# Kernel tuning notes

Hardware: AMD Instinct MI355X
Metric: run time of the kernel (lower is better)

The kernel has to match this reference:

```python
import jax, jax.numpy as jnp
import numpy as np

B, N, C = 64, 16384, 3
NUM_PATCHES, PATCH_POINTS, EMBED_DIM = 64, 32, 384
BN_EPS = 1e-5


def farthest_point_sample(xyz, npoint):
    # xyz: (B, N, 3) -> (B, npoint) int32 indices. Deterministic start at index 0
    # (torch version uses a random start point).
    b, n, _ = xyz.shape
    bidx = jnp.arange(b)

    def step(carry, _):
        distance, farthest = carry
        centroid = xyz[bidx, farthest][:, None, :]          # (B,1,3)
        d = jnp.sum((xyz - centroid) ** 2, -1)              # (B,N)
        distance = jnp.minimum(distance, d)
        nxt = jnp.argmax(distance, -1).astype(jnp.int32)
        return (distance, nxt), farthest

    init = (jnp.full((b, n), 1e10, xyz.dtype), jnp.zeros((b,), jnp.int32))
    _, cent = jax.lax.scan(step, init, None, length=npoint)
    return jnp.transpose(cent)                               # (B, npoint)


def query_ball(xyz, new_xyz, nsample):
    # nsample nearest neighbors by squared distance (radius arg is unused in source).
    sq = (jnp.sum(new_xyz ** 2, -1)[:, :, None]
          + jnp.sum(xyz ** 2, -1)[:, None, :]
          - 2.0 * jnp.einsum('bsc,bnc->bsn', new_xyz, xyz))  # (B,S,N)
    _, idx = jax.lax.top_k(-sq, nsample)                     # smallest distances
    return idx                                               # (B,S,K)


def batchnorm(h, g, b):
    # training-mode BN over (batch*patches, points) per channel (last axis)
    m = jnp.mean(h, axis=(0, 1, 2))
    v = jnp.mean((h - m) ** 2, axis=(0, 1, 2))
    return (h - m) * jax.lax.rsqrt(v + BN_EPS) * g + b


def setup_inputs() -> dict:
    key = jax.random.key(0)
    ks = jax.random.split(key, 4)
    x = jax.random.normal(ks[0], (B, N, C), jnp.float32)
    W1 = jax.random.normal(ks[1], (64, C), jnp.float32) * (1.0 / np.sqrt(C))
    W2 = jax.random.normal(ks[2], (128, 64), jnp.float32) * (1.0 / np.sqrt(64))
    W3 = jax.random.normal(ks[3], (EMBED_DIM, 128), jnp.float32) * (1.0 / np.sqrt(128))
    return dict(
        x=x,
        W1=W1, b1=jnp.zeros((64,), jnp.float32),
        g1=jnp.ones((64,), jnp.float32), be1=jnp.zeros((64,), jnp.float32),
        W2=W2, b2=jnp.zeros((128,), jnp.float32),
        g2=jnp.ones((128,), jnp.float32), be2=jnp.zeros((128,), jnp.float32),
        W3=W3, b3=jnp.zeros((EMBED_DIM,), jnp.float32),
    )


def reference(x, W1, b1, g1, be1, W2, b2, g2, be2, W3, b3):
    b = x.shape[0]
    bidx2 = jnp.arange(b)[:, None]
    bidx3 = jnp.arange(b)[:, None, None]

    fps_idx = farthest_point_sample(x[:, :, :3], NUM_PATCHES)   # (B,S)
    centers = x[bidx2, fps_idx][:, :, :3]                       # (B,S,3)
    idx = query_ball(x[:, :, :3], centers, PATCH_POINTS)        # (B,S,K)
    patches = x[bidx3, idx]                                     # (B,S,K,C)
    patches = jnp.concatenate(
        [patches[..., :3] - centers[:, :, None, :], patches[..., 3:]], axis=-1)

    h = jnp.einsum('bskc,oc->bsko', patches, W1) + b1           # (B,S,K,64)
    h = jax.nn.relu(batchnorm(h, g1, be1))
    h = jnp.einsum('bsko,po->bskp', h, W2) + b2                 # (B,S,K,128)
    h = jax.nn.relu(batchnorm(h, g2, be2))
    h = jnp.einsum('bskp,ep->bske', h, W3) + b3                 # (B,S,K,384)
    embeddings = jnp.max(h, axis=2)                             # (B,S,384)
    return embeddings, centers
```

## Files before the change

### kernel.cpp

```cpp
#include <hip/hip_runtime.h>
#include <hip/hip_bf16.h>

#define B_  64
#define N_  16384
#define S_  64
#define K_  32
#define C1_ 64
#define C2_ 128
#define C3_ 384
#define R_  (B_*S_*K_)
#define BN_EPS_ 1e-5f

#define PATCH_OFF 0
#define CENT_OFF  (R_*3)
#define NB1_ 512
#define P1_OFF    (CENT_OFF + B_*S_*3)
#define SC1_OFF   (P1_OFF + NB1_*C1_*2)
#define NB2_ 512
#define P2_OFF    (SC1_OFF + 2*C1_)
#define SC2_OFF   (P2_OFF + NB2_*C2_*2)
#define W2BF_OFF  (SC2_OFF + 2*C2_)
#define W3BF_OFF  (W2BF_OFF + 4096)

#define MOMB_ 48

typedef short bf16x8 __attribute__((ext_vector_type(8)));
typedef float f32x4  __attribute__((ext_vector_type(4)));

static __device__ __forceinline__ unsigned short f2bf(float f) {
  unsigned u = __float_as_uint(f);
  unsigned r = (u + 0x7fffu + ((u >> 16) & 1u)) >> 16;
  return (unsigned short)r;
}

static __device__ __forceinline__ unsigned fToKey(float d) {
  unsigned u = __float_as_uint(d);
  return (u & 0x80000000u) ? ~u : (u | 0x80000000u);
}
static __device__ __forceinline__ float keyToF(unsigned k) {
  return (k & 0x80000000u) ? __uint_as_float(k & 0x7fffffffu)
                           : -__uint_as_float(~k);
}

__global__ void prep_kernel(const float* __restrict__ W2, const float* __restrict__ W3,
                            short* __restrict__ w2bf, short* __restrict__ w3bf) {
  int i = blockIdx.x * 256 + threadIdx.x;
  if (i < C2_*C1_) w2bf[i] = (short)f2bf(W2[i]);
  int j = i - C2_*C1_;
  if (j >= 0 && j < C3_*C2_) w3bf[j] = (short)f2bf(W3[j]);
}

__global__ __launch_bounds__(1024, 4) void fps_kernel(const float* __restrict__ x,
        float* __restrict__ centers, float* __restrict__ outCent) {
  int b = blockIdx.x;
  int t = threadIdx.x;
  const float* xb = x + (size_t)b * N_ * 3;
  float px[16], py[16], pz[16], dist[16];
#pragma unroll
  for (int j = 0; j < 16; ++j) {
    int n = j * 1024 + t;
    px[j] = xb[n*3+0]; py[j] = xb[n*3+1]; pz[j] = xb[n*3+2];
    dist[j] = 1e10f;
  }
  __shared__ float wd[2][16];
  __shared__ int   wi[2][16];
  float cx = xb[0], cy = xb[1], cz = xb[2];
  int lane = t & 63, wv = t >> 6;
  for (int s = 0; s < S_; ++s) {
    if (t == 0) {
      int task = b * S_ + s;
      centers[task*3+0] = cx; centers[task*3+1] = cy; centers[task*3+2] = cz;
      outCent[task*3+0] = cx; outCent[task*3+1] = cy; outCent[task*3+2] = cz;
    }
    float bd = -1.0f; int bn = 0;
#pragma unroll
    for (int j = 0; j < 16; ++j) {
      float dx = px[j]-cx, dy = py[j]-cy, dz = pz[j]-cz;
      float d = __builtin_fmaf(dz, dz, __builtin_fmaf(dy, dy, dx*dx));
      float dm = fminf(dist[j], d);
      dist[j] = dm;
      int n = j*1024 + t;
      if (dm > bd) { bd = dm; bn = n; }
    }
#pragma unroll
    for (int m = 1; m < 64; m <<= 1) {
      float od = __shfl_xor(bd, m, 64); int on = __shfl_xor(bn, m, 64);
      if (od > bd || (od == bd && on < bn)) { bd = od; bn = on; }
    }
    int buf = s & 1;
    if (lane == 0) { wd[buf][wv] = bd; wi[buf][wv] = bn; }
    __syncthreads();
    float vd = wd[buf][lane & 15];
    int   vi = wi[buf][lane & 15];
#pragma unroll
    for (int m = 1; m < 16; m <<= 1) {
      float od = __shfl_xor(vd, m, 64); int oi = __shfl_xor(vi, m, 64);
      if (od > vd || (od == vd && oi < vi)) { vd = od; vi = oi; }
    }
    int gn = vi;
    cx = xb[gn*3+0]; cy = xb[gn*3+1]; cz = xb[gn*3+2];
  }
}

__global__ __launch_bounds__(1024, 8) void qb_kernel(const float* __restrict__ x,
        const float* __restrict__ centers, float* __restrict__ patches) {
  int t = threadIdx.x;
  int lane = t & 63, wv = t >> 6;
  int task = blockIdx.x;
  int b = task >> 6;
  const float* xb = x + (size_t)b * N_ * 3;
  float cx = centers[task*3+0], cy = centers[task*3+1], cz = centers[task*3+2];
  float A = __builtin_fmaf(cz, cz, __builtin_fmaf(cy, cy, cx*cx));

  __shared__ unsigned long long wbuf[16][64];
  __shared__ unsigned long long tour[512];
  __shared__ int winIdx[32];
  __shared__ int sortedIdx[32];

  unsigned key[16];
  unsigned kmin = 0xffffffffu;
  int base = wv * 1024;
#pragma unroll
  for (int j = 0; j < 16; ++j) {
    int n = base + j*64 + lane;
    float qx = xb[n*3+0], qy = xb[n*3+1], qz = xb[n*3+2];
    float Bn = __builtin_fmaf(qz, qz, __builtin_fmaf(qy, qy, qx*qx));
    float dt = __builtin_fmaf(cz, qz, __builtin_fmaf(cy, qy, cx*qx));
    float d  = __builtin_fmaf(-2.0f, dt, A + Bn);
    unsigned k = fToKey(d);
    key[j] = k;
    kmin = min(kmin, k);
  }
  unsigned ksam = key[0];
#pragma unroll
  for (int m = 1; m < 64; m <<= 1) {
    kmin = min(kmin, (unsigned)__shfl_xor((int)kmin, m, 64));
    ksam = min(ksam, (unsigned)__shfl_xor((int)ksam, m, 64));
  }

  auto wcount = [&](unsigned T) -> int {
    int cc = 0;
#pragma unroll
    for (int j = 0; j < 16; ++j) cc += (key[j] < T) ? 1 : 0;
#pragma unroll
    for (int m = 1; m < 64; m <<= 1) cc += __shfl_xor(cc, m, 64);
    return cc;
  };

  unsigned Tcur = ksam;
  int c = wcount(Tcur);
  float dmin = keyToF(kmin);
  for (int iter = 0; iter < 4 && !(c >= 32 && c <= 64); ++iter) {
    float dcur = keyToF(Tcur);
    if (!(dcur > dmin)) break;
    float f = 48.0f / fmaxf((float)c, 2.0f);
    float ratio = exp2f(0.66666667f * log2f(f));
    float dnew = dmin + (dcur - dmin) * ratio;
    unsigned Tn = fToKey(dnew);
    if (Tn == Tcur) break;
    Tcur = Tn;
    c = wcount(Tcur);
  }

  int cw = 0;
  bool ok = (c >= 32 && c <= 64);
  if (!ok) {
    unsigned a = 0xffffffffu, o = 0u;
#pragma unroll
    for (int j = 0; j < 16; ++j) { a &= key[j]; o |= key[j]; }
#pragma unroll
    for (int m = 1; m < 64; m <<= 1) {
      a &= (unsigned)__shfl_xor((int)a, m, 64);
      o |= (unsigned)__shfl_xor((int)o, m, 64);
    }
    unsigned diff = a ^ o, result = 0u;
    bool early = false;
    for (int bit = 31; bit >= 0; --bit) {
      unsigned msk = 1u << bit;
      if (!(diff & msk)) { result |= (a & msk); continue; }
      unsigned tryv = result | msk;
      int cc = wcount(tryv);
      if (cc >= 32 && cc <= 64) { early = true; Tcur = tryv; break; }
      if (cc < 32) result = tryv;
    }
    if (early) {
      ok = true;
    } else {
      unsigned Tx = result;
      int bpos = 0;
#pragma unroll
      for (int j = 0; j < 16; ++j) {
        bool p = key[j] < Tx;
        unsigned long long mk = __ballot(p);
        if (p) {
          int pos = bpos + (int)__popcll(mk & ((1ull << lane) - 1ull));
          wbuf[wv][pos] = ((unsigned long long)key[j] << 32) | (unsigned)(base + j*64 + lane);
        }
        bpos += (int)__popcll(mk);
      }
      int cl = bpos;
      int need = 32 - cl;
      int picked = -1;
      for (int r = 0; r < need; ++r) {
        int candn = 0x7fffffff;
#pragma unroll
        for (int j = 0; j < 16; ++j) {
          int n = base + j*64 + lane;
          if (key[j] == Tx && n > picked && n < candn) candn = n;
        }
#pragma unroll
        for (int m = 1; m < 64; m <<= 1) candn = min(candn, __shfl_xor(candn, m, 64));
        if (lane == 0)
          wbuf[wv][cl + r] = ((unsigned long long)Tx << 32) | (unsigned)candn;
        picked = candn;
      }
      cw = 32;
    }
  }
  if (ok) {
    int bpos = 0;
#pragma unroll
    for (int j = 0; j < 16; ++j) {
      bool p = key[j] < Tcur;
      unsigned long long mk = __ballot(p);
      if (p) {
        int pos = bpos + (int)__popcll(mk & ((1ull << lane) - 1ull));
        wbuf[wv][pos] = ((unsigned long long)key[j] << 32) | (unsigned)(base + j*64 + lane);
      }
      bpos += (int)__popcll(mk);
    }
    cw = bpos;
  }

  {
    unsigned long long me = (lane < cw) ? wbuf[wv][lane] : ~0ull;
    int rk = 0;
    for (int jj = 0; jj < cw; ++jj) rk += (wbuf[wv][jj] < me) ? 1 : 0;
    if (lane < cw && rk < 32) tour[wv*32 + rk] = me;
  }
  __syncthreads();

  if (t < 512) {
    unsigned long long me = tour[t];
    int rk = 0;
    for (int jj = 0; jj < 512; ++jj) rk += (tour[jj] < me) ? 1 : 0;
    if (rk < 32) winIdx[rk] = (int)(me & 0xffffffffu);
  }
  __syncthreads();
  if (t < 32) {
    int v = winIdx[t];
    int slot = 0;
#pragma unroll
    for (int j = 0; j < 32; ++j) slot += (winIdx[j] < v) ? 1 : 0;
    sortedIdx[slot] = v;
  }
  __syncthreads();
  if (t < 32) {
    int n = sortedIdx[t];
    float qx = xb[n*3+0], qy = xb[n*3+1], qz = xb[n*3+2];
    size_t row = (size_t)task * K_ + t;
    patches[row*3+0] = qx - cx;
    patches[row*3+1] = qy - cy;
    patches[row*3+2] = qz - cz;
  }
}

__global__ __launch_bounds__(256) void mom_kernel(const float* __restrict__ patches,
        float* __restrict__ mom) {
  int t = threadIdx.x;
  float s[9] = {0,0,0,0,0,0,0,0,0};
  for (int r = blockIdx.x*256 + t; r < R_; r += MOMB_*256) {
    const float* p = patches + (size_t)r*3;
    float x0 = p[0], y0 = p[1], z0 = p[2];
    s[0] += x0; s[1] += y0; s[2] += z0;
    s[3] += x0*x0; s[4] += y0*y0; s[5] += z0*z0;
    s[6] += x0*y0; s[7] += x0*z0; s[8] += y0*z0;
  }
  __shared__ float red[4][9];
  int lane = t & 63, wv = t >> 6;
#pragma unroll
  for (int k = 0; k < 9; ++k) {
    float v = s[k];
#pragma unroll
    for (int m = 1; m < 64; m <<= 1) v += __shfl_xor(v, m, 64);
    if (lane == 0) red[wv][k] = v;
  }
  __syncthreads();
  if (t < 9) mom[blockIdx.x*9 + t] = red[0][t] + red[1][t] + red[2][t] + red[3][t];
}

__global__ void finalize1_kernel(const float* __restrict__ mom,
        const float* __restrict__ W1, const float* __restrict__ b1,
        const float* __restrict__ g, const float* __restrict__ be,
        float* __restrict__ scale, float* __restrict__ shift) {
  int o = threadIdx.x;
  __shared__ double M[9];
  if (o < 9) {
    double ss = 0.0;
    for (int i = 0; i < MOMB_; ++i) ss += (double)mom[i*9 + o];
    M[o] = ss;
  }
  __syncthreads();
  if (o >= C1_) return;
  double w0 = W1[o*3], w1 = W1[o*3+1], w2 = W1[o*3+2], bb = b1[o];
  double wSp = w0*M[0] + w1*M[1] + w2*M[2];
  double s1 = wSp + (double)R_*bb;
  double s2 = w0*w0*M[3] + w1*w1*M[4] + w2*w2*M[5]
            + 2.0*(w0*w1*M[6] + w0*w2*M[7] + w1*w2*M[8])
            + 2.0*bb*wSp + (double)R_*bb*bb;
  float m   = (float)(s1 / (double)R_);
  float eh2 = (float)(s2 / (double)R_);
  float v = eh2 - m*m;
  float rs = rsqrtf(v + BN_EPS_);
  float sc = g[o] * rs;
  scale[o] = sc;
  shift[o] = be[o] - m*sc;
}

__global__ void finalize_kernel(const float* __restrict__ part, int nblk, int nch,
        const float* __restrict__ g, const float* __restrict__ be,
        const float* __restrict__ bias,
        float* __restrict__ scale, float* __restrict__ shift) {
  int o = threadIdx.x;
  if (o >= nch) return;
  double s1 = 0.0, s2 = 0.0;
  for (int i = 0; i < nblk; ++i) {
    s1 += (double)part[i*nch*2 + o*2 + 0];
    s2 += (double)part[i*nch*2 + o*2 + 1];
  }
  float m   = (float)(s1 / (double)R_);
  float eh2 = (float)(s2 / (double)R_);
  float v = eh2 - m*m;
  float rs = rsqrtf(v + BN_EPS_);
  float sc = g[o] * rs;
  scale[o] = sc;
  float sh = be[o] - m*sc;
  if (bias) sh += bias[o]*sc;
  shift[o] = sh;
}

__global__ __launch_bounds__(256) void stats2_kernel(const float* __restrict__ patches,
        const float* __restrict__ W1, const float* __restrict__ b1,
        const float* __restrict__ sc1, const float* __restrict__ sh1,
        const float* __restrict__ W2, const float* __restrict__ b2,
        float* __restrict__ part) {
  __shared__ float a1L[128][68];
  __shared__ float red[2][128][2];
  int t = threadIdx.x;
  float4 wreg[16];
  const float4* w2r = (const float4*)(W2 + (t & 127)*64);
#pragma unroll
  for (int c = 0; c < 16; ++c) wreg[c] = w2r[c];
  float bb = b2[t & 127];
  float s1 = 0.f, s2 = 0.f;
  int rg = t >> 7;
  for (int tile = 0; tile < 2; ++tile) {
    int r0 = blockIdx.x * 256 + tile * 128;
    {
      int r = t & 127, oh = t >> 7;
      const float* p = patches + (size_t)(r0 + r) * 3;
      float p0 = p[0], p1 = p[1], p2 = p[2];
#pragma unroll
      for (int j = 0; j < 32; ++j) {
        int o = oh*32 + j;
        float h = p0*W1[o*3] + p1*W1[o*3+1] + p2*W1[o*3+2] + b1[o];
        a1L[r][o] = fmaxf(h*sc1[o] + sh1[o], 0.f);
      }
    }
    __syncthreads();
    for (int i = 0; i < 64; ++i) {
      int r = rg*64 + i;
      float acc = bb;
      const float4* a4 = (const float4*)(&a1L[r][0]);
#pragma unroll
      for (int c = 0; c < 16; ++c) {
        float4 a = a4[c];
        acc += a.x*wreg[c].x; acc += a.y*wreg[c].y;
        acc += a.z*wreg[c].z; acc += a.w*wreg[c].w;
      }
      s1 += acc; s2 += acc*acc;
    }
    __syncthreads();
  }
  red[rg][t & 127][0] = s1; red[rg][t & 127][1] = s2;
  __syncthreads();
  if (t < 128) {
    part[blockIdx.x*256 + t*2 + 0] = red[0][t][0] + red[1][t][0];
    part[blockIdx.x*256 + t*2 + 1] = red[0][t][1] + red[1][t][1];
  }
}

__global__ __launch_bounds__(256) void embed_kernel(
        const float* __restrict__ patches,
        const float* __restrict__ W1, const float* __restrict__ b1,
        const float* __restrict__ sc1, const float* __restrict__ sh1,
        const short* __restrict__ w2bf, const float* __restrict__ sc2,
        const float* __restrict__ sh2f,
        const short* __restrict__ w3bf, const float* __restrict__ b3,
        float* __restrict__ out) {
  __shared__ char lds[49152];
  int t = threadIdx.x;
  int l = t & 63, w = t >> 6;
  int lo = l & 15, hi = l >> 4;

  {
    int row = t >> 1, half = t & 1;
    const float* p = patches + ((size_t)blockIdx.x*128 + row)*3;
    float p0 = p[0], p1 = p[1], p2 = p[2];
    int swz = (row & 7) << 4;
    char* dst = lds + row*128;
#pragma unroll
    for (int g = 0; g < 4; ++g) {
      unsigned short pk[8];
#pragma unroll
      for (int j = 0; j < 8; ++j) {
        int o = half*32 + g*8 + j;
        float h = p0*W1[o*3] + p1*W1[o*3+1] + p2*W1[o*3+2] + b1[o];
        pk[j] = f2bf(fmaxf(h*sc1[o] + sh1[o], 0.f));
      }
      int4 v;
      v.x = pk[0] | (pk[1]<<16); v.y = pk[2] | (pk[3]<<16);
      v.z = pk[4] | (pk[5]<<16); v.w = pk[6] | (pk[7]<<16);
      *(int4*)(dst + (((half*64 + g*16)) ^ swz)) = v;
    }
  }
  __syncthreads();

  {
    bf16x8 af[2][2];
#pragma unroll
    for (int mt = 0; mt < 2; ++mt) {
      int row = w*32 + mt*16 + lo;
#pragma unroll
      for (int ks = 0; ks < 2; ++ks)
        af[mt][ks] = *(const bf16x8*)(lds + row*128 + ((ks*64 + hi*16) ^ ((row&7)<<4)));
    }
#pragma unroll
    for (int nt = 0; nt < 8; ++nt) {
      f32x4 acc0 = {0.f,0.f,0.f,0.f}, acc1 = {0.f,0.f,0.f,0.f};
      int n = nt*16 + lo;
#pragma unroll
      for (int ks = 0; ks < 2; ++ks) {
        bf16x8 bfv = *(const bf16x8*)(w2bf + n*64 + ks*32 + hi*8);
        acc0 = __builtin_amdgcn_mfma_f32_16x16x32_bf16(af[0][ks], bfv, acc0, 0, 0, 0);
        acc1 = __builtin_amdgcn_mfma_f32_16x16x32_bf16(af[1][ks], bfv, acc1, 0, 0, 0);
      }
      float sc = sc2[n], sh = sh2f[n];
#pragma unroll
      for (int mt = 0; mt < 2; ++mt) {
        f32x4 c = mt ? acc1 : acc0;
#pragma unroll
        for (int r = 0; r < 4; ++r) {
          int row = w*32 + mt*16 + hi*4 + r;
          unsigned short v = f2bf(fmaxf(c[r]*sc + sh, 0.f));
          *(short*)(lds + 16384 + row*256 + ((n*2) ^ ((row&7)<<4))) = (short)v;
        }
      }
    }
  }
  __syncthreads();

  {
    bf16x8 af[2][4];
#pragma unroll
    for (int mt = 0; mt < 2; ++mt) {
      int row = w*32 + mt*16 + lo;
#pragma unroll
      for (int ks = 0; ks < 4; ++ks)
        af[mt][ks] = *(const bf16x8*)(lds + 16384 + row*256 + ((ks*64 + hi*16) ^ ((row&7)<<4)));
    }
    size_t gtask = (size_t)blockIdx.x*4 + w;
#pragma unroll 4
    for (int nt = 0; nt < 24; ++nt) {
      f32x4 acc0 = {0.f,0.f,0.f,0.f}, acc1 = {0.f,0.f,0.f,0.f};
      int e = nt*16 + lo;
#pragma unroll
      for (int ks = 0; ks < 4; ++ks) {
        bf16x8 bfv = *(const bf16x8*)(w3bf + e*128 + ks*32 + hi*8);
        acc0 = __builtin_amdgcn_mfma_f32_16x16x32_bf16(af[0][ks], bfv, acc0, 0, 0, 0);
        acc1 = __builtin_amdgcn_mfma_f32_16x16x32_bf16(af[1][ks], bfv, acc1, 0, 0, 0);
      }
      float m0 = fmaxf(fmaxf(acc0[0], acc0[1]), fmaxf(acc0[2], acc0[3]));
      float m1 = fmaxf(fmaxf(acc1[0], acc1[1]), fmaxf(acc1[2], acc1[3]));
      float m = fmaxf(m0, m1);
      m = fmaxf(m, __shfl_xor(m, 16, 64));
      m = fmaxf(m, __shfl_xor(m, 32, 64));
      if (l < 16) out[gtask*C3_ + e] = m + b3[e];
    }
  }
}

extern "C" void kernel_launch(void* const* d_in, const int* in_sizes, int n_in,
                              void* d_out, int out_size, void* d_ws, size_t ws_size,
                              hipStream_t stream) {
  (void)in_sizes; (void)n_in; (void)out_size; (void)ws_size;
  const float* x   = (const float*)d_in[0];
  const float* W1  = (const float*)d_in[1];
  const float* b1  = (const float*)d_in[2];
  const float* g1  = (const float*)d_in[3];
  const float* be1 = (const float*)d_in[4];
  const float* W2  = (const float*)d_in[5];
  const float* b2  = (const float*)d_in[6];
  const float* g2  = (const float*)d_in[7];
  const float* be2 = (const float*)d_in[8];
  const float* W3  = (const float*)d_in[9];
  const float* b3  = (const float*)d_in[10];
  float* out = (float*)d_out;
  float* ws  = (float*)d_ws;

  float* patches = ws + PATCH_OFF;
  float* centers = ws + CENT_OFF;
  float* mom1    = ws + P1_OFF;
  float* sc1     = ws + SC1_OFF; float* sh1 = sc1 + C1_;
  float* part2   = ws + P2_OFF;
  float* sc2     = ws + SC2_OFF; float* sh2 = sc2 + C2_;
  short* w2bf    = (short*)(ws + W2BF_OFF);
  short* w3bf    = (short*)(ws + W3BF_OFF);
  float* outCent = out + (size_t)B_*S_*C3_;

  prep_kernel<<<dim3((C2_*C1_ + C3_*C2_)/256), dim3(256), 0, stream>>>(W2, W3, w2bf, w3bf);
  fps_kernel<<<dim3(B_), dim3(1024), 0, stream>>>(x, centers, outCent);
  qb_kernel<<<dim3(4096), dim3(1024), 0, stream>>>(x, centers, patches);
  mom_kernel<<<dim3(MOMB_), dim3(256), 0, stream>>>(patches, mom1);
  finalize1_kernel<<<dim3(1), dim3(64), 0, stream>>>(mom1, W1, b1, g1, be1, sc1, sh1);
  stats2_kernel<<<dim3(NB2_), dim3(256), 0, stream>>>(patches, W1, b1, sc1, sh1, W2, b2, part2);
  finalize_kernel<<<dim3(1), dim3(128), 0, stream>>>(part2, NB2_, C2_, g2, be2, b2, sc2, sh2);
  embed_kernel<<<dim3(1024), dim3(256), 0, stream>>>(patches, W1, b1, sc1, sh1,
                                                     w2bf, sc2, sh2, w3bf, b3, out);
}
```

Baseline: 666.9 us.

## Fuse BN1 moment reduction into query-ball kernel and speed up tournament rank

The separate moment kernel is removed. Each query-ball block now reduces its 32 patch points' first and second moments by wave shuffle and writes them to a per-task buffer, and finalize1 reduces the 4096 partials with 576 threads. The final 512-way rank count is replaced by pruning against the minimum of the per-wave 32nd elements plus binary searches over the 16 sorted segments. This removes one launch and a re-read of the patches, and cuts the O(512) comparisons per thread. In exchange, finalize1 now has more partials to sum.

```diff
diff --git a/kernel.cpp b/kernel.cpp
--- a/kernel.cpp
+++ b/kernel.cpp
@@ -13,16 +13,13 @@
 
 #define PATCH_OFF 0
 #define CENT_OFF  (R_*3)
-#define NB1_ 512
 #define P1_OFF    (CENT_OFF + B_*S_*3)
-#define SC1_OFF   (P1_OFF + NB1_*C1_*2)
+#define SC1_OFF   (P1_OFF + 65536)
 #define NB2_ 512
 #define P2_OFF    (SC1_OFF + 2*C1_)
 #define SC2_OFF   (P2_OFF + NB2_*C2_*2)
 #define W2BF_OFF  (SC2_OFF + 2*C2_)
 #define W3BF_OFF  (W2BF_OFF + 4096)
-
-#define MOMB_ 48
 
 typedef short bf16x8 __attribute__((ext_vector_type(8)));
 typedef float f32x4  __attribute__((ext_vector_type(4)));
@@ -103,7 +100,8 @@
 }
 
 __global__ __launch_bounds__(1024, 8) void qb_kernel(const float* __restrict__ x,
-        const float* __restrict__ centers, float* __restrict__ patches) {
+        const float* __restrict__ centers, float* __restrict__ patches,
+        float* __restrict__ mom) {
   int t = threadIdx.x;
   int lane = t & 63, wv = t >> 6;
   int task = blockIdx.x;
@@ -242,9 +240,26 @@
 
   if (t < 512) {
     unsigned long long me = tour[t];
-    int rk = 0;
-    for (int jj = 0; jj < 512; ++jj) rk += (tour[jj] < me) ? 1 : 0;
-    if (rk < 32) winIdx[rk] = (int)(me & 0xffffffffu);
+    unsigned long long Tstar = tour[31];
+#pragma unroll
+    for (int w = 1; w < 16; ++w) {
+      unsigned long long v = tour[w*32 + 31];
+      if (v < Tstar) Tstar = v;
+    }
+    if (me <= Tstar) {
+      int rk = 0;
+#pragma unroll
+      for (int w = 0; w < 16; ++w) {
+        const unsigned long long* seg = &tour[w*32];
+        int pos = 0;
+#pragma unroll
+        for (int s = 32; s > 0; s >>= 1) {
+          if (pos + s <= 32 && seg[pos + s - 1] < me) pos += s;
+        }
+        rk += pos;
+      }
+      if (rk < 32) winIdx[rk] = (int)(me & 0xffffffffu);
+    }
   }
   __syncthreads();
   if (t < 32) {
@@ -257,50 +272,46 @@
   __syncthreads();
   if (t < 32) {
     int n = sortedIdx[t];
-    float qx = xb[n*3+0], qy = xb[n*3+1], qz = xb[n*3+2];
+    float qx = xb[n*3+0] - cx, qy = xb[n*3+1] - cy, qz = xb[n*3+2] - cz;
     size_t row = (size_t)task * K_ + t;
-    patches[row*3+0] = qx - cx;
-    patches[row*3+1] = qy - cy;
-    patches[row*3+2] = qz - cz;
-  }
-}
-
-__global__ __launch_bounds__(256) void mom_kernel(const float* __restrict__ patches,
-        float* __restrict__ mom) {
-  int t = threadIdx.x;
-  float s[9] = {0,0,0,0,0,0,0,0,0};
-  for (int r = blockIdx.x*256 + t; r < R_; r += MOMB_*256) {
-    const float* p = patches + (size_t)r*3;
-    float x0 = p[0], y0 = p[1], z0 = p[2];
-    s[0] += x0; s[1] += y0; s[2] += z0;
-    s[3] += x0*x0; s[4] += y0*y0; s[5] += z0*z0;
-    s[6] += x0*y0; s[7] += x0*z0; s[8] += y0*z0;
-  }
-  __shared__ float red[4][9];
-  int lane = t & 63, wv = t >> 6;
-#pragma unroll
-  for (int k = 0; k < 9; ++k) {
-    float v = s[k];
-#pragma unroll
-    for (int m = 1; m < 64; m <<= 1) v += __shfl_xor(v, m, 64);
-    if (lane == 0) red[wv][k] = v;
-  }
-  __syncthreads();
-  if (t < 9) mom[blockIdx.x*9 + t] = red[0][t] + red[1][t] + red[2][t] + red[3][t];
-}
-
-__global__ void finalize1_kernel(const float* __restrict__ mom,
+    patches[row*3+0] = qx;
+    patches[row*3+1] = qy;
+    patches[row*3+2] = qz;
+    float mv[9];
+    mv[0]=qx; mv[1]=qy; mv[2]=qz;
+    mv[3]=qx*qx; mv[4]=qy*qy; mv[5]=qz*qz;
+    mv[6]=qx*qy; mv[7]=qx*qz; mv[8]=qy*qz;
+#pragma unroll
+    for (int k = 0; k < 9; ++k) {
+      float v = mv[k];
+#pragma unroll
+      for (int m = 1; m < 32; m <<= 1) v += __shfl_xor(v, m, 64);
+      if (t == 0) mom[(size_t)task*9 + k] = v;
+    }
+  }
+}
+
+__global__ __launch_bounds__(576) void finalize1_kernel(const float* __restrict__ mom,
         const float* __restrict__ W1, const float* __restrict__ b1,
         const float* __restrict__ g, const float* __restrict__ be,
         float* __restrict__ scale, float* __restrict__ shift) {
-  int o = threadIdx.x;
+  int t = threadIdx.x;
+  __shared__ float part[64][9];
+  if (t < 576) {
+    int gp = t / 9, k = t % 9;
+    float s = 0.f;
+    for (int i = gp; i < 4096; i += 64) s += mom[(size_t)i*9 + k];
+    part[gp][k] = s;
+  }
+  __syncthreads();
   __shared__ double M[9];
-  if (o < 9) {
+  if (t < 9) {
     double ss = 0.0;
-    for (int i = 0; i < MOMB_; ++i) ss += (double)mom[i*9 + o];
-    M[o] = ss;
-  }
-  __syncthreads();
+    for (int g2 = 0; g2 < 64; ++g2) ss += (double)part[g2][t];
+    M[t] = ss;
+  }
+  __syncthreads();
+  int o = t;
   if (o >= C1_) return;
   double w0 = W1[o*3], w1 = W1[o*3+1], w2 = W1[o*3+2], bb = b1[o];
   double wSp = w0*M[0] + w1*M[1] + w2*M[2];
@@ -520,9 +531,8 @@
 
   prep_kernel<<<dim3((C2_*C1_ + C3_*C2_)/256), dim3(256), 0, stream>>>(W2, W3, w2bf, w3bf);
   fps_kernel<<<dim3(B_), dim3(1024), 0, stream>>>(x, centers, outCent);
-  qb_kernel<<<dim3(4096), dim3(1024), 0, stream>>>(x, centers, patches);
-  mom_kernel<<<dim3(MOMB_), dim3(256), 0, stream>>>(patches, mom1);
-  finalize1_kernel<<<dim3(1), dim3(64), 0, stream>>>(mom1, W1, b1, g1, be1, sc1, sh1);
+  qb_kernel<<<dim3(4096), dim3(1024), 0, stream>>>(x, centers, patches, mom1);
+  finalize1_kernel<<<dim3(1), dim3(576), 0, stream>>>(mom1, W1, b1, g1, be1, sc1, sh1);
   stats2_kernel<<<dim3(NB2_), dim3(256), 0, stream>>>(patches, W1, b1, sc1, sh1, W2, b2, part2);
   finalize_kernel<<<dim3(1), dim3(128), 0, stream>>>(part2, NB2_, C2_, g2, be2, b2, sc2, sh2);
   embed_kernel<<<dim3(1024), dim3(256), 0, stream>>>(patches, W1, b1, sc1, sh1,
```

After: 661.7 us. Within noise of the previous version (-0.8%).
